# Optimization experiments

Hardware: AMD Instinct MI355X
Metric: run time of the kernel (lower is better)

## Reference

```python
import jax, jax.numpy as jnp
import numpy as np

N_HEADS = 16
ROPE_BASE = 10000.0


def _rope_tables(T, head_dim):
    inv_freq = 1.0 / (ROPE_BASE ** (jnp.arange(0, head_dim, 2, dtype=jnp.float32) / head_dim))
    freqs = jnp.outer(jnp.arange(T, dtype=jnp.float32), inv_freq)  # (T, head_dim/2)
    emb = jnp.concatenate([freqs, freqs], axis=-1)  # (T, head_dim)
    return jnp.cos(emb), jnp.sin(emb)


def _rotate_half(u):
    u1, u2 = jnp.split(u, 2, axis=-1)
    return jnp.concatenate([-u2, u1], axis=-1)


def setup_inputs() -> dict:
    key = jax.random.key(0)
    k1, k2, k3 = jax.random.split(key, 3)
    B, T, D = 2, 2048, 1024
    x = jax.random.normal(k1, (B, T, D), dtype=jnp.float32)
    W_qkv = jax.random.normal(k2, (D, 3 * D), dtype=jnp.float32) * (1.0 / np.sqrt(D))
    W_out = jax.random.normal(k3, (D, D), dtype=jnp.float32) * (1.0 / np.sqrt(D))
    return {"x": x, "W_qkv": W_qkv, "W_out": W_out}


def reference(x, W_qkv, W_out):
    B, T, D = x.shape
    H = N_HEADS
    Dh = D // H
    # fused QKV projection
    qkv = (x @ W_qkv).reshape(B, T, 3, H, Dh)
    q = jnp.transpose(qkv[:, :, 0], (0, 2, 1, 3))  # (B,H,T,Dh)
    k = jnp.transpose(qkv[:, :, 1], (0, 2, 1, 3))
    v = jnp.transpose(qkv[:, :, 2], (0, 2, 1, 3))
    # RoPE
    cos, sin = _rope_tables(T, Dh)  # (T, Dh), broadcasts over (B,H)
    q = q * cos + _rotate_half(q) * sin
    k = k * cos + _rotate_half(k) * sin
    # causal SDPA
    scale = 1.0 / jnp.sqrt(jnp.asarray(Dh, dtype=x.dtype))
    scores = jnp.einsum('bhqd,bhkd->bhqk', q, k) * scale
    causal = jnp.tril(jnp.ones((T, T), dtype=bool))
    scores = jnp.where(causal, scores, jnp.asarray(-jnp.inf, dtype=scores.dtype))
    attn = jax.nn.softmax(scores, axis=-1)
    out = jnp.einsum('bhqk,bhkd->bhqd', attn, v)
    out = jnp.transpose(out, (0, 2, 1, 3)).reshape(B, T, D)
    return out @ W_out
```

## Files before the change

### kernel.cpp

```cpp
#include <hip/hip_runtime.h>
#include <math.h>

typedef unsigned short u16;
typedef short bf16x8 __attribute__((ext_vector_type(8)));
typedef float f32x4 __attribute__((ext_vector_type(4)));

#define ROPE_SC 0.18033688011112042f

__device__ __forceinline__ u16 f2bf(float f) {
    union { float f; unsigned u; } x; x.f = f;
    unsigned u = x.u;
    unsigned r = (u + 0x7fffu + ((u >> 16) & 1u)) >> 16;
    return (u16)r;
}
__device__ __forceinline__ unsigned pack2(float a, float b) {
    return (unsigned)f2bf(a) | ((unsigned)f2bf(b) << 16);
}
__device__ __forceinline__ f32x4 mfma16(bf16x8 a, bf16x8 b, f32x4 c) {
    return __builtin_amdgcn_mfma_f32_16x16x32_bf16(a, b, c, 0, 0, 0);
}
__device__ __forceinline__ void gload_lds16(const void* g, void* l) {
    __builtin_amdgcn_global_load_lds((const __attribute__((address_space(1))) void*)g,
                                     (__attribute__((address_space(3))) void*)l,
                                     16, 0, 0);
}

__global__ void cvt_bf16(const float* __restrict__ X, u16* __restrict__ Y) {
    int i = (blockIdx.x * 256 + threadIdx.x) * 4;
    float4 v = *(const float4*)(X + i);
    uint2 o;
    o.x = pack2(v.x, v.y);
    o.y = pack2(v.z, v.w);
    *(uint2*)(Y + i) = o;
}

__global__ void transpose_cvt(const float* __restrict__ W, u16* __restrict__ Wt,
                              int R, int C) {
    __shared__ u16 tile[32][33];
    int tx = threadIdx.x & 31, ty = threadIdx.x >> 5;
    int bx = blockIdx.x * 32;
    int by = blockIdx.y * 32;
#pragma unroll
    for (int r = ty; r < 32; r += 8)
        tile[r][tx] = f2bf(W[(size_t)(by + r) * C + bx + tx]);
    __syncthreads();
#pragma unroll
    for (int r = ty; r < 32; r += 8)
        Wt[(size_t)(bx + r) * R + by + tx] = tile[tx][r];
}

__global__ void rope_tab(float* __restrict__ tab) {
    int i = blockIdx.x * 256 + threadIdx.x;
    int t = i >> 5, d = i & 31;
    float invf = powf(10000.0f, -(float)d / 32.0f);
    float ang = (float)t * invf;
    tab[i] = cosf(ang);
    tab[i + 65536] = sinf(ang);
}

__global__ __launch_bounds__(512) void gemm_qkv(const u16* __restrict__ A,
                                                const u16* __restrict__ Bt,
                                                const float* __restrict__ tab,
                                                u16* __restrict__ qb,
                                                u16* __restrict__ kb,
                                                u16* __restrict__ vt,
                                                int M, int N, int K) {
    __shared__ u16 lA[128 * 64];
    __shared__ u16 lB[128 * 64];
    const int tid = threadIdx.x;
    const int wave = tid >> 6, lane = tid & 63;
    const int l15 = lane & 15, l4 = lane >> 4;
    const int nwg = gridDim.x * gridDim.y;
    const int orig = blockIdx.y * gridDim.x + blockIdx.x;
    const int swz = (orig & 7) * (nwg >> 3) + (orig >> 3);
    const int m0 = (swz / gridDim.x) * 128, n0 = (swz % gridDim.x) * 128;
    const int wm = (wave >> 1) * 32, wn = (wave & 1) * 64;
    f32x4 acc[2][4] = {};
    for (int k0 = 0; k0 < K; k0 += 64) {
#pragma unroll
        for (int it = 0; it < 2; ++it) {
            int cb = it * 512 + wave * 64;
            int c = cb + lane;
            int r = c >> 3, s = c & 7;
            int sd = ((s ^ (r & 7)) << 3);
            gload_lds16(A + (size_t)(m0 + r) * K + k0 + sd, &lA[(size_t)cb * 8]);
            gload_lds16(Bt + (size_t)(n0 + r) * K + k0 + sd, &lB[(size_t)cb * 8]);
        }
        __syncthreads();
#pragma unroll
        for (int kk = 0; kk < 2; ++kk) {
            bf16x8 af[2], bf[4];
#pragma unroll
            for (int mi = 0; mi < 2; ++mi) {
                int row = wm + mi * 16 + l15;
                af[mi] = *(const bf16x8*)(&lA[row * 64 + (((kk * 4 + l4) ^ (row & 7)) << 3)]);
            }
#pragma unroll
            for (int ni = 0; ni < 4; ++ni) {
                int row = wn + ni * 16 + l15;
                bf[ni] = *(const bf16x8*)(&lB[row * 64 + (((kk * 4 + l4) ^ (row & 7)) << 3)]);
            }
#pragma unroll
            for (int mi = 0; mi < 2; ++mi)
#pragma unroll
                for (int ni = 0; ni < 4; ++ni)
                    acc[mi][ni] = mfma16(af[mi], bf[ni], acc[mi][ni]);
        }
        __syncthreads();
    }
    const int colg = n0 + wn;
    const int region = colg >> 10;
    const int h = (colg & 1023) >> 6;
    if (region == 2) {
#pragma unroll
        for (int mi = 0; mi < 2; ++mi) {
            int t0 = m0 + wm + mi * 16 + l4 * 4;
            int b = t0 >> 11, tq0 = t0 & 2047;
#pragma unroll
            for (int ni = 0; ni < 4; ++ni) {
                int dcol = ni * 16 + l15;
                uint2 pk;
                pk.x = pack2(acc[mi][ni][0], acc[mi][ni][1]);
                pk.y = pack2(acc[mi][ni][2], acc[mi][ni][3]);
                *(uint2*)(vt + ((size_t)(b * 16 + h) * 64 + dcol) * 2048 + tq0) = pk;
            }
        }
    } else {
        const float sc = (region == 0) ? ROPE_SC : 1.0f;
        u16* dst = (region == 0) ? qb : kb;
#pragma unroll
        for (int mi = 0; mi < 2; ++mi)
#pragma unroll
            for (int i = 0; i < 4; ++i) {
                int t = m0 + wm + mi * 16 + l4 * 4 + i;
                int b = t >> 11, tq = t & 2047;
                const float* tcb = tab + tq * 32;
                const float* tsb = tab + 65536 + tq * 32;
                size_t base = ((size_t)(b * 16 + h) * 2048 + tq) * 64;
#pragma unroll
                for (int ni = 0; ni < 2; ++ni) {
                    int d32 = ni * 16 + l15;
                    float cs = tcb[d32], sn = tsb[d32];
                    float a = acc[mi][ni][i], bb = acc[mi][ni + 2][i];
                    dst[base + d32]      = f2bf((a * cs - bb * sn) * sc);
                    dst[base + d32 + 32] = f2bf((bb * cs + a * sn) * sc);
                }
            }
    }
}

__global__ __launch_bounds__(512) void gemm_bt_n64(const u16* __restrict__ A,
                                                   const u16* __restrict__ Bt,
                                                   float* __restrict__ C,
                                                   int M, int N, int K) {
    __shared__ u16 lA[128 * 64];
    __shared__ u16 lB[64 * 64];
    const int tid = threadIdx.x;
    const int wave = tid >> 6, lane = tid & 63;
    const int l15 = lane & 15, l4 = lane >> 4;
    const int nwg = gridDim.x * gridDim.y;
    const int orig = blockIdx.y * gridDim.x + blockIdx.x;
    const int swz = (orig & 7) * (nwg >> 3) + (orig >> 3);
    const int m0 = (swz / gridDim.x) * 128, n0 = (swz % gridDim.x) * 64;
    const int wm = (wave >> 1) * 32, wn = (wave & 1) * 32;
    f32x4 acc[2][2] = {};
    for (int k0 = 0; k0 < K; k0 += 64) {
#pragma unroll
        for (int it = 0; it < 2; ++it) {
            int cb = it * 512 + wave * 64;
            int c = cb + lane;
            int r = c >> 3, s = c & 7;
            int sd = ((s ^ (r & 7)) << 3);
            gload_lds16(A + (size_t)(m0 + r) * K + k0 + sd, &lA[(size_t)cb * 8]);
        }
        {
            int cb = wave * 64;
            int c = cb + lane;
            int r = c >> 3, s = c & 7;
            int sd = ((s ^ (r & 7)) << 3);
            gload_lds16(Bt + (size_t)(n0 + r) * K + k0 + sd, &lB[(size_t)cb * 8]);
        }
        __syncthreads();
#pragma unroll
        for (int kk = 0; kk < 2; ++kk) {
            bf16x8 af[2], bf[2];
#pragma unroll
            for (int mi = 0; mi < 2; ++mi) {
                int row = wm + mi * 16 + l15;
                af[mi] = *(const bf16x8*)(&lA[row * 64 + (((kk * 4 + l4) ^ (row & 7)) << 3)]);
            }
#pragma unroll
            for (int ni = 0; ni < 2; ++ni) {
                int row = wn + ni * 16 + l15;
                bf[ni] = *(const bf16x8*)(&lB[row * 64 + (((kk * 4 + l4) ^ (row & 7)) << 3)]);
            }
#pragma unroll
            for (int mi = 0; mi < 2; ++mi)
#pragma unroll
                for (int ni = 0; ni < 2; ++ni)
                    acc[mi][ni] = mfma16(af[mi], bf[ni], acc[mi][ni]);
        }
        __syncthreads();
    }
#pragma unroll
    for (int mi = 0; mi < 2; ++mi)
#pragma unroll
        for (int ni = 0; ni < 2; ++ni)
#pragma unroll
            for (int i = 0; i < 4; ++i) {
                int r = m0 + wm + mi * 16 + l4 * 4 + i;
                int cc = n0 + wn + ni * 16 + l15;
                C[(size_t)r * N + cc] = acc[mi][ni][i];
            }
}

__global__ __launch_bounds__(256, 4) void flash14(const u16* __restrict__ qb,
                                                  const u16* __restrict__ kb,
                                                  const u16* __restrict__ vt,
                                                  u16* __restrict__ ao) {
    __shared__ u16 lK[2][64 * 64];
    __shared__ u16 lV[2][64 * 64];
    const int orig = blockIdx.x;
    const int xcd = orig & 7, p = orig >> 3;
    const int cup = p & 31, layer = p >> 5;
    const int bh = xcd * 4 + layer;
    const int qt = (layer & 1) ? cup : 31 - cup;
    const int b = bh >> 4, h = bh & 15;
    const int tid = threadIdx.x;
    const int wave = tid >> 6, lane = tid & 63;
    const int l15 = lane & 15, l4 = lane >> 4;
    const u16* qptr = qb + (size_t)bh * 2048 * 64;
    const u16* kptr = kb + (size_t)bh * 2048 * 64;
    const u16* vptr = vt + (size_t)bh * 64 * 2048;

    const int qrow = qt * 64 + wave * 16 + l15;
    bf16x8 q0 = *(const bf16x8*)(qptr + (size_t)qrow * 64 + l4 * 8);
    bf16x8 q1 = *(const bf16x8*)(qptr + (size_t)qrow * 64 + 32 + l4 * 8);

    f32x4 O[4] = {};
    f32x4 lacc = {};
    float mrun = -INFINITY;

    bf16x8 onesf;
#pragma unroll
    for (int j = 0; j < 8; ++j) onesf[j] = (short)0x3F80;

    int idxO[4];
#pragma unroll
    for (int i = 0; i < 4; ++i) idxO[i] = (lane & 48) | (l4 * 4 + i);

    const int r0q = ((l15 >> 2) << 3) | (l15 & 3);

    auto stage = [&](int buf, int kv0) {
#pragma unroll
        for (int it = 0; it < 2; ++it) {
            int cb = wave * 64 + it * 256;
            int c = cb + lane;
            int r = c >> 3, s = c & 7;
            int fK = (r & 3) | ((r >> 1) & 4);
            gload_lds16(kptr + (size_t)(kv0 + r) * 64 + ((s ^ fK) << 3), &lK[buf][cb * 8]);
            gload_lds16(vptr + (size_t)r * 2048 + kv0 + ((s ^ (r & 7)) << 3), &lV[buf][cb * 8]);
        }
    };
    auto ldK = [&](int buf, int row, int slot) -> bf16x8 {
        int f = (row & 3) | ((row >> 1) & 4);
        return *(const bf16x8*)(&lK[buf][row * 64 + ((slot ^ f) << 3)]);
    };
    auto ldV = [&](int buf, int row, int slot) -> bf16x8 {
        return *(const bf16x8*)(&lV[buf][row * 64 + ((slot ^ (row & 7)) << 3)]);
    };

    auto smpack = [&](f32x4 S[4], float& mr, f32x4& la, f32x4 Ov[4],
                      bf16x8 af[2], bool diag, int kv0, int qr) {
        float p2[4][4];
#pragma unroll
        for (int m = 0; m < 4; ++m)
#pragma unroll
            for (int i = 0; i < 4; ++i) {
                float s = S[m][i];
                if (diag && (kv0 + ((m >> 1) << 5) + (l4 << 3) + ((m & 1) << 2) + i > qr))
                    s = -INFINITY;
                p2[m][i] = s;
            }
        float m = p2[0][0];
#pragma unroll
        for (int c = 0; c < 4; ++c)
#pragma unroll
            for (int i = 0; i < 4; ++i) m = fmaxf(m, p2[c][i]);
        m = fmaxf(m, __shfl_xor(m, 16));
        m = fmaxf(m, __shfl_xor(m, 32));
        if (__any(m > mr)) {
            float mnew = fmaxf(mr, m);
            float corr = __builtin_amdgcn_exp2f(mr - mnew);
            mr = mnew;
            f32x4 cfv;
#pragma unroll
            for (int i = 0; i < 4; ++i) cfv[i] = __shfl(corr, idxO[i]);
            Ov[0] *= cfv; Ov[1] *= cfv; Ov[2] *= cfv; Ov[3] *= cfv;
            la *= cfv;
        }
#pragma unroll
        for (int c = 0; c < 4; ++c)
#pragma unroll
            for (int i = 0; i < 4; ++i)
                p2[c][i] = __builtin_amdgcn_exp2f(p2[c][i] - mr);
        unsigned w[4][2];
#pragma unroll
        for (int c = 0; c < 4; ++c) {
            asm("v_cvt_pk_bf16_f32 %0, %1, %2" : "=v"(w[c][0]) : "v"(p2[c][0]), "v"(p2[c][1]));
            asm("v_cvt_pk_bf16_f32 %0, %1, %2" : "=v"(w[c][1]) : "v"(p2[c][2]), "v"(p2[c][3]));
        }
#pragma unroll
        for (int ks = 0; ks < 2; ++ks) {
            union { unsigned u[4]; bf16x8 v; } cvt;
            cvt.u[0] = w[2 * ks][0];
            cvt.u[1] = w[2 * ks][1];
            cvt.u[2] = w[2 * ks + 1][0];
            cvt.u[3] = w[2 * ks + 1][1];
            af[ks] = cvt.v;
        }
        la = mfma16(af[0], onesf, la);
        la = mfma16(af[1], onesf, la);
    };

    stage(0, 0);
    for (int kvb = 0; kvb <= qt; ++kvb) {
        const int cur = kvb & 1;
        const int kv0 = kvb * 64;
        if (kvb < qt) {
            stage(cur ^ 1, kv0 + 64);
            asm volatile("s_waitcnt vmcnt(4)" ::: "memory");
        } else {
            asm volatile("s_waitcnt vmcnt(0)" ::: "memory");
        }
        __builtin_amdgcn_s_barrier();
        __builtin_amdgcn_sched_barrier(0);

        f32x4 S[4] = {};
#pragma unroll
        for (int mm = 0; mm < 4; ++mm) {
            int row = r0q + ((mm >> 1) << 5) + ((mm & 1) << 2);
            bf16x8 kf0 = ldK(cur, row, l4);
            bf16x8 kf1 = ldK(cur, row, 4 + l4);
            S[mm] = mfma16(kf0, q0, S[mm]);
            S[mm] = mfma16(kf1, q1, S[mm]);
        }
        bf16x8 af[2];
        smpack(S, mrun, lacc, O, af, kvb == qt, kv0, qrow);
#pragma unroll
        for (int ks = 0; ks < 2; ++ks)
#pragma unroll
            for (int c2 = 0; c2 < 4; ++c2) {
                bf16x8 vf = ldV(cur, c2 * 16 + l15, ks * 4 + l4);
                O[c2] = mfma16(af[ks], vf, O[c2]);
            }
        __builtin_amdgcn_s_barrier();
    }

#pragma unroll
    for (int i = 0; i < 4; ++i) {
        float rcp = 1.f / lacc[i];
        int qg = qt * 64 + wave * 16 + l4 * 4 + i;
#pragma unroll
        for (int c2 = 0; c2 < 4; ++c2)
            ao[(size_t)(b * 2048 + qg) * 1024 + h * 64 + c2 * 16 + l15] = f2bf(O[c2][i] * rcp);
    }
}

extern "C" void kernel_launch(void* const* d_in, const int* in_sizes, int n_in,
                              void* d_out, int out_size, void* d_ws, size_t ws_size,
                              hipStream_t stream) {
    const float* x    = (const float*)d_in[0];
    const float* Wqkv = (const float*)d_in[1];
    const float* Wout = (const float*)d_in[2];
    float* out = (float*)d_out;
    char* ws = (char*)d_ws;

    u16*   xb  = (u16*)(ws + 0);
    u16*   Wtq = (u16*)(ws + 8388608);
    u16*   Wto = (u16*)(ws + 14680064);
    u16*   qb  = (u16*)(ws + 67108864);
    u16*   kb  = (u16*)(ws + 75497472);
    u16*   vt  = (u16*)(ws + 83886080);
    float* tab = (float*)(ws + 92274688);
    u16*   ao  = (u16*)(ws + 0);

    cvt_bf16<<<dim3(4096), dim3(256), 0, stream>>>(x, xb);
    transpose_cvt<<<dim3(96, 32), dim3(256), 0, stream>>>(Wqkv, Wtq, 1024, 3072);
    transpose_cvt<<<dim3(32, 32), dim3(256), 0, stream>>>(Wout, Wto, 1024, 1024);
    rope_tab<<<dim3(256), dim3(256), 0, stream>>>(tab);
    gemm_qkv<<<dim3(24, 32), dim3(512), 0, stream>>>(xb, Wtq, tab, qb, kb, vt, 4096, 3072, 1024);
    flash14<<<dim3(1024), dim3(256), 0, stream>>>(qb, kb, vt, ao);
    gemm_bt_n64<<<dim3(16, 32), dim3(512), 0, stream>>>(ao, Wto, out, 4096, 1024, 1024);
}
```

Baseline: 105.9 us.

## Halve flash query tile to 32 rows and load V straight into registers

The attention kernel now uses 128-thread blocks covering 32 query rows each, with twice as many blocks and a remapped causal work order. V tiles are no longer staged in LDS; each wave reads its V fragments straight from global memory into registers at the top of each KV iteration. Only K stays double-buffered in LDS, and the vmcnt waits are adjusted to account for the extra outstanding loads. The goal is better load balance and occupancy with less LDS, at the cost of less K/V reuse per block and more global/L2 traffic for V.

```diff
diff --git a/kernel.cpp b/kernel.cpp
--- a/kernel.cpp
+++ b/kernel.cpp
@@ -214,26 +214,26 @@
             }
 }
 
-__global__ __launch_bounds__(256, 4) void flash14(const u16* __restrict__ qb,
+__global__ __launch_bounds__(128, 4) void flash15(const u16* __restrict__ qb,
                                                   const u16* __restrict__ kb,
                                                   const u16* __restrict__ vt,
                                                   u16* __restrict__ ao) {
     __shared__ u16 lK[2][64 * 64];
-    __shared__ u16 lV[2][64 * 64];
     const int orig = blockIdx.x;
     const int xcd = orig & 7, p = orig >> 3;
-    const int cup = p & 31, layer = p >> 5;
+    const int layer = p & 3, idx = p >> 2;
     const int bh = xcd * 4 + layer;
-    const int qt = (layer & 1) ? cup : 31 - cup;
+    const int qt = (layer & 1) ? idx : 63 - idx;
     const int b = bh >> 4, h = bh & 15;
     const int tid = threadIdx.x;
     const int wave = tid >> 6, lane = tid & 63;
     const int l15 = lane & 15, l4 = lane >> 4;
+    const int niter = (qt >> 1) + 1;
     const u16* qptr = qb + (size_t)bh * 2048 * 64;
     const u16* kptr = kb + (size_t)bh * 2048 * 64;
     const u16* vptr = vt + (size_t)bh * 64 * 2048;
 
-    const int qrow = qt * 64 + wave * 16 + l15;
+    const int qrow = qt * 32 + wave * 16 + l15;
     bf16x8 q0 = *(const bf16x8*)(qptr + (size_t)qrow * 64 + l4 * 8);
     bf16x8 q1 = *(const bf16x8*)(qptr + (size_t)qrow * 64 + 32 + l4 * 8);
 
@@ -253,21 +253,17 @@
 
     auto stage = [&](int buf, int kv0) {
 #pragma unroll
-        for (int it = 0; it < 2; ++it) {
-            int cb = wave * 64 + it * 256;
+        for (int it = 0; it < 4; ++it) {
+            int cb = it * 128 + wave * 64;
             int c = cb + lane;
             int r = c >> 3, s = c & 7;
             int fK = (r & 3) | ((r >> 1) & 4);
             gload_lds16(kptr + (size_t)(kv0 + r) * 64 + ((s ^ fK) << 3), &lK[buf][cb * 8]);
-            gload_lds16(vptr + (size_t)r * 2048 + kv0 + ((s ^ (r & 7)) << 3), &lV[buf][cb * 8]);
         }
     };
     auto ldK = [&](int buf, int row, int slot) -> bf16x8 {
         int f = (row & 3) | ((row >> 1) & 4);
         return *(const bf16x8*)(&lK[buf][row * 64 + ((slot ^ f) << 3)]);
-    };
-    auto ldV = [&](int buf, int row, int slot) -> bf16x8 {
-        return *(const bf16x8*)(&lV[buf][row * 64 + ((slot ^ (row & 7)) << 3)]);
     };
 
     auto smpack = [&](f32x4 S[4], float& mr, f32x4& la, f32x4 Ov[4],
@@ -324,14 +320,23 @@
     };
 
     stage(0, 0);
-    for (int kvb = 0; kvb <= qt; ++kvb) {
+    for (int kvb = 0; kvb < niter; ++kvb) {
         const int cur = kvb & 1;
         const int kv0 = kvb * 64;
-        if (kvb < qt) {
+
+        bf16x8 vf[2][4];
+#pragma unroll
+        for (int ks = 0; ks < 2; ++ks)
+#pragma unroll
+            for (int c2 = 0; c2 < 4; ++c2)
+                vf[ks][c2] = *(const bf16x8*)(vptr + (size_t)(c2 * 16 + l15) * 2048
+                                              + kv0 + (ks * 4 + l4) * 8);
+
+        if (kvb < niter - 1) {
             stage(cur ^ 1, kv0 + 64);
-            asm volatile("s_waitcnt vmcnt(4)" ::: "memory");
+            asm volatile("s_waitcnt vmcnt(12)" ::: "memory");
         } else {
-            asm volatile("s_waitcnt vmcnt(0)" ::: "memory");
+            asm volatile("s_waitcnt vmcnt(8)" ::: "memory");
         }
         __builtin_amdgcn_s_barrier();
         __builtin_amdgcn_sched_barrier(0);
@@ -346,21 +351,19 @@
             S[mm] = mfma16(kf1, q1, S[mm]);
         }
         bf16x8 af[2];
-        smpack(S, mrun, lacc, O, af, kvb == qt, kv0, qrow);
+        smpack(S, mrun, lacc, O, af, kvb == niter - 1, kv0, qrow);
 #pragma unroll
         for (int ks = 0; ks < 2; ++ks)
 #pragma unroll
-            for (int c2 = 0; c2 < 4; ++c2) {
-                bf16x8 vf = ldV(cur, c2 * 16 + l15, ks * 4 + l4);
-                O[c2] = mfma16(af[ks], vf, O[c2]);
-            }
+            for (int c2 = 0; c2 < 4; ++c2)
+                O[c2] = mfma16(af[ks], vf[ks][c2], O[c2]);
         __builtin_amdgcn_s_barrier();
     }
 
 #pragma unroll
     for (int i = 0; i < 4; ++i) {
         float rcp = 1.f / lacc[i];
-        int qg = qt * 64 + wave * 16 + l4 * 4 + i;
+        int qg = qt * 32 + wave * 16 + l4 * 4 + i;
 #pragma unroll
         for (int c2 = 0; c2 < 4; ++c2)
             ao[(size_t)(b * 2048 + qg) * 1024 + h * 64 + c2 * 16 + l15] = f2bf(O[c2][i] * rcp);
@@ -390,6 +393,6 @@
     transpose_cvt<<<dim3(32, 32), dim3(256), 0, stream>>>(Wout, Wto, 1024, 1024);
     rope_tab<<<dim3(256), dim3(256), 0, stream>>>(tab);
     gemm_qkv<<<dim3(24, 32), dim3(512), 0, stream>>>(xb, Wtq, tab, qb, kb, vt, 4096, 3072, 1024);
-    flash14<<<dim3(1024), dim3(256), 0, stream>>>(qb, kb, vt, ao);
+    flash15<<<dim3(2048), dim3(128), 0, stream>>>(qb, kb, vt, ao);
     gemm_bt_n64<<<dim3(16, 32), dim3(512), 0, stream>>>(ao, Wto, out, 4096, 1024, 1024);
 }
```

After: 147.8 us. +39.5%, slower.

## Rewrite QKV GEMM with 256x256 tiles and double-buffered ping-pong pipeline

Applied to the files above, without the earlier changes.

Replaces the 128x128-tile QKV projection GEMM with a 256x256-tile kernel. It double-buffers LDS and splits each k-step into four sub-phases that interleave LDS fragment loads and async global-to-LDS prefetch of the next stage with MFMA bursts. The bursts are run at raised wave priority, with explicit barriers and waitcnts. The aim is to raise arithmetic intensity per tile and hide global load latency behind compute. In exchange, the grid shrinks to 192 workgroups, fewer than the CU count, and LDS use grows to 128 KB, which limits occupancy to one block per CU.

```diff
diff --git a/kernel.cpp b/kernel.cpp
--- a/kernel.cpp
+++ b/kernel.cpp
@@ -58,62 +58,155 @@
     tab[i + 65536] = sinf(ang);
 }
 
-__global__ __launch_bounds__(512) void gemm_qkv(const u16* __restrict__ A,
-                                                const u16* __restrict__ Bt,
-                                                const float* __restrict__ tab,
-                                                u16* __restrict__ qb,
-                                                u16* __restrict__ kb,
-                                                u16* __restrict__ vt,
-                                                int M, int N, int K) {
-    __shared__ u16 lA[128 * 64];
-    __shared__ u16 lB[128 * 64];
+__global__ __launch_bounds__(512, 2) void gemm_qkv2(const u16* __restrict__ A,
+                                                    const u16* __restrict__ Bt,
+                                                    const float* __restrict__ tab,
+                                                    u16* __restrict__ qb,
+                                                    u16* __restrict__ kb,
+                                                    u16* __restrict__ vt) {
+    __shared__ u16 lA[2][256 * 64];
+    __shared__ u16 lB[2][256 * 64];
+    const int K = 1024;
     const int tid = threadIdx.x;
     const int wave = tid >> 6, lane = tid & 63;
     const int l15 = lane & 15, l4 = lane >> 4;
     const int nwg = gridDim.x * gridDim.y;
     const int orig = blockIdx.y * gridDim.x + blockIdx.x;
     const int swz = (orig & 7) * (nwg >> 3) + (orig >> 3);
-    const int m0 = (swz / gridDim.x) * 128, n0 = (swz % gridDim.x) * 128;
-    const int wm = (wave >> 1) * 32, wn = (wave & 1) * 64;
-    f32x4 acc[2][4] = {};
-    for (int k0 = 0; k0 < K; k0 += 64) {
-#pragma unroll
-        for (int it = 0; it < 2; ++it) {
-            int cb = it * 512 + wave * 64;
-            int c = cb + lane;
-            int r = c >> 3, s = c & 7;
-            int sd = ((s ^ (r & 7)) << 3);
-            gload_lds16(A + (size_t)(m0 + r) * K + k0 + sd, &lA[(size_t)cb * 8]);
-            gload_lds16(Bt + (size_t)(n0 + r) * K + k0 + sd, &lB[(size_t)cb * 8]);
-        }
-        __syncthreads();
-#pragma unroll
-        for (int kk = 0; kk < 2; ++kk) {
-            bf16x8 af[2], bf[4];
-#pragma unroll
-            for (int mi = 0; mi < 2; ++mi) {
+    const int m0 = (swz / gridDim.x) * 256, n0 = (swz % gridDim.x) * 256;
+    const int wm = (wave >> 2) * 128, wn = (wave & 3) * 64;
+
+    f32x4 acc[8][4] = {};
+
+    auto stageHalf = [&](int s2, int j) {
+        int buf = s2 & 1;
+        int rb = (j & 1) * 128;
+#pragma unroll
+        for (int e = 0; e < 2; ++e) {
+            int cb = wave * 128 + e * 64;
+            int chunk = cb + lane;
+            int r = rb + (chunk >> 3);
+            int sl = chunk & 7;
+            int sd = ((sl ^ (r & 7)) << 3);
+            if (j < 2)
+                gload_lds16(A + (size_t)(m0 + r) * K + s2 * 64 + sd,
+                            &lA[buf][rb * 64 + cb * 8]);
+            else
+                gload_lds16(Bt + (size_t)(n0 + r) * K + s2 * 64 + sd,
+                            &lB[buf][rb * 64 + cb * 8]);
+        }
+    };
+
+#pragma unroll
+    for (int j = 0; j < 4; ++j) stageHalf(0, j);
+    asm volatile("s_waitcnt vmcnt(0)" ::: "memory");
+    __builtin_amdgcn_s_barrier();
+
+    bf16x8 af[4][2], b01[2][2], b23[2][2];
+
+    for (int s = 0; s < 16; ++s) {
+        const int buf = s & 1;
+#pragma unroll
+        for (int mi = 0; mi < 4; ++mi)
+#pragma unroll
+            for (int kk = 0; kk < 2; ++kk) {
                 int row = wm + mi * 16 + l15;
-                af[mi] = *(const bf16x8*)(&lA[row * 64 + (((kk * 4 + l4) ^ (row & 7)) << 3)]);
-            }
-#pragma unroll
-            for (int ni = 0; ni < 4; ++ni) {
-                int row = wn + ni * 16 + l15;
-                bf[ni] = *(const bf16x8*)(&lB[row * 64 + (((kk * 4 + l4) ^ (row & 7)) << 3)]);
-            }
-#pragma unroll
-            for (int mi = 0; mi < 2; ++mi)
-#pragma unroll
-                for (int ni = 0; ni < 4; ++ni)
-                    acc[mi][ni] = mfma16(af[mi], bf[ni], acc[mi][ni]);
-        }
-        __syncthreads();
+                af[mi][kk] = *(const bf16x8*)(&lA[buf][row * 64 + (((kk * 4 + l4) ^ (row & 7)) << 3)]);
+            }
+#pragma unroll
+        for (int nb = 0; nb < 2; ++nb)
+#pragma unroll
+            for (int kk = 0; kk < 2; ++kk) {
+                int row = wn + nb * 16 + l15;
+                b01[nb][kk] = *(const bf16x8*)(&lB[buf][row * 64 + (((kk * 4 + l4) ^ (row & 7)) << 3)]);
+            }
+        if (s < 15) { stageHalf(s + 1, 0); stageHalf(s + 1, 1); }
+        __builtin_amdgcn_s_barrier();
+        asm volatile("s_waitcnt lgkmcnt(0)" ::: "memory");
+        __builtin_amdgcn_sched_barrier(0);
+        __builtin_amdgcn_s_setprio(1);
+#pragma unroll
+        for (int mi = 0; mi < 4; ++mi)
+#pragma unroll
+            for (int nb = 0; nb < 2; ++nb)
+#pragma unroll
+                for (int kk = 0; kk < 2; ++kk)
+                    acc[mi][nb] = mfma16(af[mi][kk], b01[nb][kk], acc[mi][nb]);
+        __builtin_amdgcn_s_setprio(0);
+        __builtin_amdgcn_s_barrier();
+
+#pragma unroll
+        for (int nb = 0; nb < 2; ++nb)
+#pragma unroll
+            for (int kk = 0; kk < 2; ++kk) {
+                int row = wn + 32 + nb * 16 + l15;
+                b23[nb][kk] = *(const bf16x8*)(&lB[buf][row * 64 + (((kk * 4 + l4) ^ (row & 7)) << 3)]);
+            }
+        if (s < 15) { stageHalf(s + 1, 2); stageHalf(s + 1, 3); }
+        __builtin_amdgcn_s_barrier();
+        asm volatile("s_waitcnt lgkmcnt(0)" ::: "memory");
+        __builtin_amdgcn_sched_barrier(0);
+        __builtin_amdgcn_s_setprio(1);
+#pragma unroll
+        for (int mi = 0; mi < 4; ++mi)
+#pragma unroll
+            for (int nb = 0; nb < 2; ++nb)
+#pragma unroll
+                for (int kk = 0; kk < 2; ++kk)
+                    acc[mi][2 + nb] = mfma16(af[mi][kk], b23[nb][kk], acc[mi][2 + nb]);
+        __builtin_amdgcn_s_setprio(0);
+        __builtin_amdgcn_s_barrier();
+
+#pragma unroll
+        for (int mi = 0; mi < 4; ++mi)
+#pragma unroll
+            for (int kk = 0; kk < 2; ++kk) {
+                int row = wm + 64 + mi * 16 + l15;
+                af[mi][kk] = *(const bf16x8*)(&lA[buf][row * 64 + (((kk * 4 + l4) ^ (row & 7)) << 3)]);
+            }
+        __builtin_amdgcn_s_barrier();
+        asm volatile("s_waitcnt lgkmcnt(0)" ::: "memory");
+        __builtin_amdgcn_sched_barrier(0);
+        __builtin_amdgcn_s_setprio(1);
+#pragma unroll
+        for (int mi = 0; mi < 4; ++mi)
+#pragma unroll
+            for (int nb = 0; nb < 2; ++nb)
+#pragma unroll
+                for (int kk = 0; kk < 2; ++kk)
+                    acc[4 + mi][2 + nb] = mfma16(af[mi][kk], b23[nb][kk], acc[4 + mi][2 + nb]);
+        __builtin_amdgcn_s_setprio(0);
+        __builtin_amdgcn_s_barrier();
+
+#pragma unroll
+        for (int nb = 0; nb < 2; ++nb)
+#pragma unroll
+            for (int kk = 0; kk < 2; ++kk) {
+                int row = wn + nb * 16 + l15;
+                b01[nb][kk] = *(const bf16x8*)(&lB[buf][row * 64 + (((kk * 4 + l4) ^ (row & 7)) << 3)]);
+            }
+        __builtin_amdgcn_s_barrier();
+        asm volatile("s_waitcnt lgkmcnt(0)" ::: "memory");
+        __builtin_amdgcn_sched_barrier(0);
+        __builtin_amdgcn_s_setprio(1);
+#pragma unroll
+        for (int mi = 0; mi < 4; ++mi)
+#pragma unroll
+            for (int nb = 0; nb < 2; ++nb)
+#pragma unroll
+                for (int kk = 0; kk < 2; ++kk)
+                    acc[4 + mi][nb] = mfma16(af[mi][kk], b01[nb][kk], acc[4 + mi][nb]);
+        __builtin_amdgcn_s_setprio(0);
+        asm volatile("s_waitcnt vmcnt(0)" ::: "memory");
+        __builtin_amdgcn_s_barrier();
     }
+
     const int colg = n0 + wn;
     const int region = colg >> 10;
     const int h = (colg & 1023) >> 6;
     if (region == 2) {
 #pragma unroll
-        for (int mi = 0; mi < 2; ++mi) {
+        for (int mi = 0; mi < 8; ++mi) {
             int t0 = m0 + wm + mi * 16 + l4 * 4;
             int b = t0 >> 11, tq0 = t0 & 2047;
 #pragma unroll
@@ -129,7 +222,7 @@
         const float sc = (region == 0) ? ROPE_SC : 1.0f;
         u16* dst = (region == 0) ? qb : kb;
 #pragma unroll
-        for (int mi = 0; mi < 2; ++mi)
+        for (int mi = 0; mi < 8; ++mi)
 #pragma unroll
             for (int i = 0; i < 4; ++i) {
                 int t = m0 + wm + mi * 16 + l4 * 4 + i;
@@ -389,7 +482,7 @@
     transpose_cvt<<<dim3(96, 32), dim3(256), 0, stream>>>(Wqkv, Wtq, 1024, 3072);
     transpose_cvt<<<dim3(32, 32), dim3(256), 0, stream>>>(Wout, Wto, 1024, 1024);
     rope_tab<<<dim3(256), dim3(256), 0, stream>>>(tab);
-    gemm_qkv<<<dim3(24, 32), dim3(512), 0, stream>>>(xb, Wtq, tab, qb, kb, vt, 4096, 3072, 1024);
+    gemm_qkv2<<<dim3(12, 16), dim3(512), 0, stream>>>(xb, Wtq, tab, qb, kb, vt);
     flash14<<<dim3(1024), dim3(256), 0, stream>>>(qb, kb, vt, ao);
     gemm_bt_n64<<<dim3(16, 32), dim3(512), 0, stream>>>(ao, Wto, out, 4096, 1024, 1024);
 }
```

Result: slower. 114.7 us (+8.3%).
